# Performance work log

Hardware: AMD Instinct MI355X
Metric: run time of the kernel (lower is better)

Reference implementation:

```python
import jax, jax.numpy as jnp
import numpy as np

EPS = 1e-12  # torch F.normalize clamp
D = 4        # max_displacement


def _l2norm_c(x):
    # L2 normalize over channel dim (axis=1), matching F.normalize(p=2, dim=1)
    n = jnp.sqrt(jnp.sum(x * x, axis=1, keepdims=True))
    return x / jnp.maximum(n, EPS)


def setup_inputs() -> dict:
    key = jax.random.key(0)
    k1, k2 = jax.random.split(key)
    B, C, H, W = 4, 128, 128, 256
    feat1 = jax.random.normal(k1, (B, C, H, W), dtype=jnp.float32)
    feat2_warped = jax.random.normal(k2, (B, C, H, W), dtype=jnp.float32)
    return {"feat1": feat1, "feat2_warped": feat2_warped}


def reference(feat1, feat2_warped):
    B, C, H, W = feat1.shape
    f1 = _l2norm_c(feat1)
    f2 = _l2norm_c(feat2_warped)
    # zero-pad spatial dims by D (matches F.unfold padding=D)
    f2p = jnp.pad(f2, ((0, 0), (0, 0), (D, D), (D, D)))
    costs = []
    # fixed (2D+1)^2 = 81 displacements, row-major (dy, dx) to match unfold ordering
    for dy in range(2 * D + 1):
        for dx in range(2 * D + 1):
            shifted = jax.lax.slice(f2p, (0, 0, dy, dx), (B, C, dy + H, dx + W))
            costs.append(jnp.sum(f1 * shifted, axis=1) / C)  # (B,H,W)
    cost = jnp.stack(costs, axis=1)  # (B, 81, H, W)
    return jax.nn.leaky_relu(cost, negative_slope=0.1)
```

## Files before the change

kernel.cpp:

```cpp
#include <hip/hip_runtime.h>

#define B_ 4
#define C_ 128
#define H_ 128
#define W_ 256
#define HW_ (H_ * W_)
#define ND 81
#define TH 8
#define TW 16
#define HR 16
#define WCOL 32
#define KC 32
#define NCHUNK (C_ / KC)
#define NTHREADS 512

typedef short bf16x8 __attribute__((ext_vector_type(8)));
typedef float f32x4 __attribute__((ext_vector_type(4)));
typedef float f32x4v __attribute__((ext_vector_type(4)));
typedef unsigned int u32x4 __attribute__((ext_vector_type(4)));

__device__ __forceinline__ int swz(int px, int byteInHalf) {
    int r = px >> 1;
    int base = (r << 7) + ((px & 1) << 6) + byteInHalf;
    return base ^ ((r & 7) << 4);
}

__device__ __forceinline__ unsigned int cvt_pk_bf16(float a, float b) {
    unsigned int r;
    asm("v_cvt_pk_bf16_f32 %0, %1, %2" : "=v"(r) : "v"(a), "v"(b));
    return r;
}

__device__ __forceinline__ void dot2_sq(unsigned int u, float& ss) {
    asm("v_dot2_f32_bf16 %0, %1, %1, %0" : "+v"(ss) : "v"(u));
}

#define BARRIER()                                             \
    do {                                                      \
        asm volatile("s_waitcnt lgkmcnt(0)" ::: "memory");    \
        __builtin_amdgcn_s_barrier();                         \
    } while (0)

__global__ __launch_bounds__(NTHREADS)
void corr81_kernel(const float* __restrict__ f1g, const float* __restrict__ f2g,
                   float* __restrict__ out) {
    __shared__ __align__(16) unsigned short f2s[2][HR * WCOL * KC];
    __shared__ __align__(16) unsigned short f1s[2][TH * TW * KC];
    float* invn2 = (float*)&f2s[0][0];
    float* invn1 = (float*)&f1s[0][0];

    const int tid  = threadIdx.x;
    const int lane = tid & 63;
    const int wave = tid >> 6;
    const int col  = lane & 15;
    const int quad = lane >> 4;

    const int flat = blockIdx.x + 16 * blockIdx.y + 256 * blockIdx.z;
    const int orig = (flat & 7) * 128 + (flat >> 3);
    const int w0 = (orig & 15) * TW;
    const int h0 = ((orig >> 4) & 15) * TH;
    const int b  = orig >> 8;
    const size_t inBase = (size_t)b * C_ * HW_;

    const int g2  = tid & 7;
    const int cp2 = (tid >> 3) & 15;
    const int rq  = tid >> 7;
    const int gw2 = w0 - 4 + g2 * 4;
    const bool colok2 = (gw2 >= 0) && (gw2 < W_);

    const int g1  = tid & 3;
    const int cp1 = (tid >> 2) & 15;
    const int r1  = tid >> 6;
    const float* src1 = f1g + inBase + (size_t)(h0 + r1) * W_ + (w0 + g1 * 4);

    const int aOff = swz(wave * 16 + col, quad * 16);

    f32x4 acc[9][2];
#pragma unroll
    for (int d = 0; d < 9; ++d) {
        acc[d][0] = (f32x4)0.f;
        acc[d][1] = (f32x4)0.f;
    }

    float ss2 = 0.f, ss1 = 0.f;
    f32x4v A0[4], A1[4], B0, B1;

#define ISSUE_LOADS(kc0)                                                        \
    {                                                                           \
        _Pragma("unroll")                                                       \
        for (int i = 0; i < 4; ++i) {                                           \
            int r  = i * 4 + rq;                                                \
            int gh = h0 - 4 + r;                                                \
            if (colok2 && gh >= 0 && gh < H_) {                                 \
                const float* s = f2g + inBase + (size_t)((kc0) + cp2 * 2) * HW_ \
                                 + (size_t)gh * W_ + gw2;                       \
                A0[i] = *(const f32x4v*)s;                                      \
                A1[i] = *(const f32x4v*)(s + HW_);                              \
            } else {                                                            \
                A0[i] = (f32x4v)0.f;                                            \
                A1[i] = (f32x4v)0.f;                                            \
            }                                                                   \
        }                                                                       \
        const float* s = src1 + (size_t)((kc0) + cp1 * 2) * HW_;                \
        B0 = *(const f32x4v*)s;                                                 \
        B1 = *(const f32x4v*)(s + HW_);                                         \
    }

#define PACK_WRITE(buf)                                                         \
    {                                                                           \
        char* w2 = (char*)&f2s[(buf)][0];                                       \
        char* w1 = (char*)&f1s[(buf)][0];                                       \
        _Pragma("unroll")                                                       \
        for (int i = 0; i < 4; ++i) {                                           \
            int r = i * 4 + rq;                                                 \
            _Pragma("unroll")                                                   \
            for (int j = 0; j < 4; ++j) {                                       \
                int px = r * 32 + g2 * 4 + j;                                   \
                *(unsigned int*)(w2 + swz(px, cp2 * 4)) =                       \
                    cvt_pk_bf16(A0[i][j], A1[i][j]);                            \
            }                                                                   \
        }                                                                       \
        _Pragma("unroll")                                                       \
        for (int j = 0; j < 4; ++j) {                                           \
            int px = r1 * 16 + g1 * 4 + j;                                      \
            *(unsigned int*)(w1 + swz(px, cp1 * 4)) = cvt_pk_bf16(B0[j], B1[j]);\
        }                                                                       \
    }

#define MFMA_PHASE(buf)                                                         \
    {                                                                           \
        const char* r2 = (const char*)&f2s[(buf)][0];                           \
        const char* r1p = (const char*)&f1s[(buf)][0];                          \
        bf16x8 af = *(const bf16x8*)(r1p + aOff);                               \
        _Pragma("unroll")                                                       \
        for (int dy = 0; dy < 9; ++dy) {                                        \
            int pb = (wave + dy) * WCOL + col;                                  \
            bf16x8 b0 = *(const bf16x8*)(r2 + swz(pb, quad * 16));              \
            bf16x8 b1 = *(const bf16x8*)(r2 + swz(pb + 16, quad * 16));         \
            acc[dy][0] = __builtin_amdgcn_mfma_f32_16x16x32_bf16(af, b0, acc[dy][0], 0, 0, 0); \
            acc[dy][1] = __builtin_amdgcn_mfma_f32_16x16x32_bf16(af, b1, acc[dy][1], 0, 0, 0); \
        }                                                                       \
    }

#define NORM_PHASE(buf)                                                         \
    {                                                                           \
        const char* r2 = (const char*)&f2s[(buf)][0];                           \
        const char* r1p = (const char*)&f1s[(buf)][0];                          \
        _Pragma("unroll")                                                       \
        for (int j = 0; j < 4; ++j) {                                           \
            u32x4 v = *(const u32x4*)(r2 + swz(tid, j * 16));                   \
            dot2_sq(v[0], ss2); dot2_sq(v[1], ss2);                             \
            dot2_sq(v[2], ss2); dot2_sq(v[3], ss2);                             \
        }                                                                       \
        u32x4 v = *(const u32x4*)(r1p + swz(tid >> 2, (tid & 3) * 16));         \
        dot2_sq(v[0], ss1); dot2_sq(v[1], ss1);                                 \
        dot2_sq(v[2], ss1); dot2_sq(v[3], ss1);                                 \
    }

    ISSUE_LOADS(0);
    PACK_WRITE(0);
    ISSUE_LOADS(KC);
    BARRIER();

#pragma unroll
    for (int k = 0; k < NCHUNK; ++k) {
        const int bk = k & 1;
        MFMA_PHASE(bk);
        if (k < NCHUNK - 1) {
            PACK_WRITE(bk ^ 1);
            if (k < NCHUNK - 2) ISSUE_LOADS((k + 2) * KC);
            NORM_PHASE(bk);
        } else {
            NORM_PHASE(bk);
            invn2[tid] = 1.f / fmaxf(sqrtf(ss2), 1e-12f);
            float t1 = ss1 + __shfl_xor(ss1, 1);
            t1 += __shfl_xor(t1, 2);
            if ((tid & 3) == 0) invn1[tid >> 2] = 1.f / fmaxf(sqrtf(t1), 1e-12f);
        }
        BARRIER();
    }

    const int hOut = h0 + wave;
    float* outB = out + (size_t)b * ND * HW_ + (size_t)hOut * W_;
    const float scale = 1.f / (float)C_;

#pragma unroll
    for (int dy = 0; dy < 9; ++dy) {
        int hr = wave + dy;
#pragma unroll
        for (int t = 0; t < 2; ++t) {
            float i2 = invn2[hr * WCOL + t * 16 + col];
#pragma unroll
            for (int r = 0; r < 4; ++r) {
                int row = quad * 4 + r;
                int dx = t * 16 + col - row;
                if (dx >= 0 && dx <= 8) {
                    float v = acc[dy][t][r] * invn1[wave * 16 + row] * i2 * scale;
                    v = (v >= 0.f) ? v : 0.1f * v;
                    outB[(size_t)(dy * 9 + dx) * HW_ + (w0 + row)] = v;
                }
            }
        }
    }
#undef ISSUE_LOADS
#undef PACK_WRITE
#undef MFMA_PHASE
#undef NORM_PHASE
}

extern "C" void kernel_launch(void* const* d_in, const int* in_sizes, int n_in,
                              void* d_out, int out_size, void* d_ws, size_t ws_size,
                              hipStream_t stream) {
    const float* f1 = (const float*)d_in[0];
    const float* f2 = (const float*)d_in[1];
    float* out = (float*)d_out;
    dim3 grid(W_ / TW, H_ / TH, B_);
    corr81_kernel<<<grid, NTHREADS, 0, stream>>>(f1, f2, out);
}
```

Before: 64.18 us.

## Load one pixel per thread across 32 channels and fold norms into packing

Global loads for f2 now give each thread one pixel and all 32 channels of the chunk, replacing the old float4 loads. The thread writes a full 64-byte channel row to LDS with 16-byte stores under a new slot swizzle. Sum-of-squares for the norms is computed from registers during packing, which removes the separate LDS-reading norm phase and its extra LDS traffic. The cost is scalar global loads, which coalesce across lanes along W but issue many more load instructions and need more registers (32 floats per thread in flight). There is also a final extra barrier before the epilogue.

```diff
diff --git a/kernel.cpp b/kernel.cpp
--- a/kernel.cpp
+++ b/kernel.cpp
@@ -13,16 +13,15 @@
 #define KC 32
 #define NCHUNK (C_ / KC)
 #define NTHREADS 512
+#define BUFSZ 40960
+#define F1OFF 32768
 
 typedef short bf16x8 __attribute__((ext_vector_type(8)));
 typedef float f32x4 __attribute__((ext_vector_type(4)));
-typedef float f32x4v __attribute__((ext_vector_type(4)));
 typedef unsigned int u32x4 __attribute__((ext_vector_type(4)));
 
-__device__ __forceinline__ int swz(int px, int byteInHalf) {
-    int r = px >> 1;
-    int base = (r << 7) + ((px & 1) << 6) + byteInHalf;
-    return base ^ ((r & 7) << 4);
+__device__ __forceinline__ int slotswz(int px, int slot) {
+    return px * 64 + ((slot ^ (px & 3) ^ ((px >> 2) & 3)) * 16);
 }
 
 __device__ __forceinline__ unsigned int cvt_pk_bf16(float a, float b) {
@@ -44,10 +43,10 @@
 __global__ __launch_bounds__(NTHREADS)
 void corr81_kernel(const float* __restrict__ f1g, const float* __restrict__ f2g,
                    float* __restrict__ out) {
-    __shared__ __align__(16) unsigned short f2s[2][HR * WCOL * KC];
-    __shared__ __align__(16) unsigned short f1s[2][TH * TW * KC];
-    float* invn2 = (float*)&f2s[0][0];
-    float* invn1 = (float*)&f1s[0][0];
+    __shared__ __align__(16) char lds[2][BUFSZ];
+    char* ldsc = &lds[0][0];
+    float* invn2 = (float*)&lds[0][0];
+    float* invn1 = (float*)&lds[0][2048];
 
     const int tid  = threadIdx.x;
     const int lane = tid & 63;
@@ -60,106 +59,90 @@
     const int w0 = (orig & 15) * TW;
     const int h0 = ((orig >> 4) & 15) * TH;
     const int b  = orig >> 8;
-    const size_t inBase = (size_t)b * C_ * HW_;
-
-    const int g2  = tid & 7;
-    const int cp2 = (tid >> 3) & 15;
-    const int rq  = tid >> 7;
-    const int gw2 = w0 - 4 + g2 * 4;
-    const bool colok2 = (gw2 >= 0) && (gw2 < W_);
-
-    const int g1  = tid & 3;
-    const int cp1 = (tid >> 2) & 15;
-    const int r1  = tid >> 6;
-    const float* src1 = f1g + inBase + (size_t)(h0 + r1) * W_ + (w0 + g1 * 4);
-
-    const int aOff = swz(wave * 16 + col, quad * 16);
+    const float* f2base = f2g + (size_t)b * C_ * HW_;
+    const float* f1base = f1g + (size_t)b * C_ * HW_;
+
+    const int hh2 = tid >> 5, ww2 = tid & 31;
+    const int gh2 = h0 - 4 + hh2, gw2 = w0 - 4 + ww2;
+    const bool v2 = (gh2 >= 0) && (gh2 < H_) && (gw2 >= 0) && (gw2 < W_);
+    const int offs2 = v2 ? (gh2 * W_ + gw2) : 0;
+    int wa[4];
+#pragma unroll
+    for (int s = 0; s < 4; ++s) wa[s] = slotswz(tid, s);
+
+    const int px1w = tid >> 2, q1 = tid & 3;
+    const int offs1 = (h0 + (px1w >> 4)) * W_ + (w0 + (px1w & 15)) + q1 * 8 * HW_;
+    const int w1a = F1OFF + slotswz(px1w, q1);
+
+    const int slotr = (quad ^ (col & 3) ^ ((col >> 2) & 3)) * 16;
+    const int rb2 = wave * 2048 + col * 64 + slotr;
+    const int rb1 = F1OFF + (wave * 16 + col) * 64 + slotr;
 
     f32x4 acc[9][2];
 #pragma unroll
-    for (int d = 0; d < 9; ++d) {
-        acc[d][0] = (f32x4)0.f;
-        acc[d][1] = (f32x4)0.f;
-    }
-
-    float ss2 = 0.f, ss1 = 0.f;
-    f32x4v A0[4], A1[4], B0, B1;
-
-#define ISSUE_LOADS(kc0)                                                        \
-    {                                                                           \
-        _Pragma("unroll")                                                       \
-        for (int i = 0; i < 4; ++i) {                                           \
-            int r  = i * 4 + rq;                                                \
-            int gh = h0 - 4 + r;                                                \
-            if (colok2 && gh >= 0 && gh < H_) {                                 \
-                const float* s = f2g + inBase + (size_t)((kc0) + cp2 * 2) * HW_ \
-                                 + (size_t)gh * W_ + gw2;                       \
-                A0[i] = *(const f32x4v*)s;                                      \
-                A1[i] = *(const f32x4v*)(s + HW_);                              \
-            } else {                                                            \
-                A0[i] = (f32x4v)0.f;                                            \
-                A1[i] = (f32x4v)0.f;                                            \
-            }                                                                   \
+    for (int d = 0; d < 9; ++d) { acc[d][0] = (f32x4)0.f; acc[d][1] = (f32x4)0.f; }
+
+    f32x4 A[8] = {};
+    f32x4 F[2] = {};
+    float ss2a = 0.f, ss2b = 0.f, ss1 = 0.f;
+
+#define ISSUE_F2(kc0)                                                           \
+    if (v2) {                                                                   \
+        _Pragma("unroll")                                                       \
+        for (int c = 0; c < 32; ++c)                                            \
+            A[c >> 2][c & 3] = (f2base + (size_t)((kc0) + c) * HW_)[offs2];     \
+    }
+
+#define ISSUE_F1(kc0)                                                           \
+    {                                                                           \
+        _Pragma("unroll")                                                       \
+        for (int j = 0; j < 8; ++j)                                             \
+            F[j >> 2][j & 3] = (f1base + (size_t)((kc0) + j) * HW_)[offs1];     \
+    }
+
+#define PACK_F2(buf)                                                            \
+    {                                                                           \
+        _Pragma("unroll")                                                       \
+        for (int s = 0; s < 4; ++s) {                                           \
+            u32x4 U;                                                            \
+            U[0] = cvt_pk_bf16(A[s * 2][0], A[s * 2][1]);                       \
+            U[1] = cvt_pk_bf16(A[s * 2][2], A[s * 2][3]);                       \
+            U[2] = cvt_pk_bf16(A[s * 2 + 1][0], A[s * 2 + 1][1]);               \
+            U[3] = cvt_pk_bf16(A[s * 2 + 1][2], A[s * 2 + 1][3]);               \
+            dot2_sq(U[0], ss2a); dot2_sq(U[1], ss2b);                           \
+            dot2_sq(U[2], ss2a); dot2_sq(U[3], ss2b);                           \
+            *(u32x4*)(ldsc + (buf) * BUFSZ + wa[s]) = U;                        \
         }                                                                       \
-        const float* s = src1 + (size_t)((kc0) + cp1 * 2) * HW_;                \
-        B0 = *(const f32x4v*)s;                                                 \
-        B1 = *(const f32x4v*)(s + HW_);                                         \
-    }
-
-#define PACK_WRITE(buf)                                                         \
-    {                                                                           \
-        char* w2 = (char*)&f2s[(buf)][0];                                       \
-        char* w1 = (char*)&f1s[(buf)][0];                                       \
-        _Pragma("unroll")                                                       \
-        for (int i = 0; i < 4; ++i) {                                           \
-            int r = i * 4 + rq;                                                 \
-            _Pragma("unroll")                                                   \
-            for (int j = 0; j < 4; ++j) {                                       \
-                int px = r * 32 + g2 * 4 + j;                                   \
-                *(unsigned int*)(w2 + swz(px, cp2 * 4)) =                       \
-                    cvt_pk_bf16(A0[i][j], A1[i][j]);                            \
-            }                                                                   \
-        }                                                                       \
-        _Pragma("unroll")                                                       \
-        for (int j = 0; j < 4; ++j) {                                           \
-            int px = r1 * 16 + g1 * 4 + j;                                      \
-            *(unsigned int*)(w1 + swz(px, cp1 * 4)) = cvt_pk_bf16(B0[j], B1[j]);\
-        }                                                                       \
+    }
+
+#define PACK_F1(buf)                                                            \
+    {                                                                           \
+        u32x4 U;                                                                \
+        U[0] = cvt_pk_bf16(F[0][0], F[0][1]);                                   \
+        U[1] = cvt_pk_bf16(F[0][2], F[0][3]);                                   \
+        U[2] = cvt_pk_bf16(F[1][0], F[1][1]);                                   \
+        U[3] = cvt_pk_bf16(F[1][2], F[1][3]);                                   \
+        dot2_sq(U[0], ss1); dot2_sq(U[1], ss1);                                 \
+        dot2_sq(U[2], ss1); dot2_sq(U[3], ss1);                                 \
+        *(u32x4*)(ldsc + (buf) * BUFSZ + w1a) = U;                              \
     }
 
 #define MFMA_PHASE(buf)                                                         \
     {                                                                           \
-        const char* r2 = (const char*)&f2s[(buf)][0];                           \
-        const char* r1p = (const char*)&f1s[(buf)][0];                          \
-        bf16x8 af = *(const bf16x8*)(r1p + aOff);                               \
+        const char* rb = ldsc + (buf) * BUFSZ;                                  \
+        bf16x8 af = *(const bf16x8*)(rb + rb1);                                 \
         _Pragma("unroll")                                                       \
         for (int dy = 0; dy < 9; ++dy) {                                        \
-            int pb = (wave + dy) * WCOL + col;                                  \
-            bf16x8 b0 = *(const bf16x8*)(r2 + swz(pb, quad * 16));              \
-            bf16x8 b1 = *(const bf16x8*)(r2 + swz(pb + 16, quad * 16));         \
+            bf16x8 b0 = *(const bf16x8*)(rb + rb2 + dy * 2048);                 \
+            bf16x8 b1 = *(const bf16x8*)(rb + rb2 + dy * 2048 + 1024);          \
             acc[dy][0] = __builtin_amdgcn_mfma_f32_16x16x32_bf16(af, b0, acc[dy][0], 0, 0, 0); \
             acc[dy][1] = __builtin_amdgcn_mfma_f32_16x16x32_bf16(af, b1, acc[dy][1], 0, 0, 0); \
         }                                                                       \
     }
 
-#define NORM_PHASE(buf)                                                         \
-    {                                                                           \
-        const char* r2 = (const char*)&f2s[(buf)][0];                           \
-        const char* r1p = (const char*)&f1s[(buf)][0];                          \
-        _Pragma("unroll")                                                       \
-        for (int j = 0; j < 4; ++j) {                                           \
-            u32x4 v = *(const u32x4*)(r2 + swz(tid, j * 16));                   \
-            dot2_sq(v[0], ss2); dot2_sq(v[1], ss2);                             \
-            dot2_sq(v[2], ss2); dot2_sq(v[3], ss2);                             \
-        }                                                                       \
-        u32x4 v = *(const u32x4*)(r1p + swz(tid >> 2, (tid & 3) * 16));         \
-        dot2_sq(v[0], ss1); dot2_sq(v[1], ss1);                                 \
-        dot2_sq(v[2], ss1); dot2_sq(v[3], ss1);                                 \
-    }
-
-    ISSUE_LOADS(0);
-    PACK_WRITE(0);
-    ISSUE_LOADS(KC);
+    ISSUE_F2(0); ISSUE_F1(0);
+    PACK_F2(0);  PACK_F1(0);
+    ISSUE_F2(KC); ISSUE_F1(KC);
     BARRIER();
 
 #pragma unroll
@@ -167,18 +150,17 @@
         const int bk = k & 1;
         MFMA_PHASE(bk);
         if (k < NCHUNK - 1) {
-            PACK_WRITE(bk ^ 1);
-            if (k < NCHUNK - 2) ISSUE_LOADS((k + 2) * KC);
-            NORM_PHASE(bk);
-        } else {
-            NORM_PHASE(bk);
-            invn2[tid] = 1.f / fmaxf(sqrtf(ss2), 1e-12f);
-            float t1 = ss1 + __shfl_xor(ss1, 1);
-            t1 += __shfl_xor(t1, 2);
-            if ((tid & 3) == 0) invn1[tid >> 2] = 1.f / fmaxf(sqrtf(t1), 1e-12f);
+            PACK_F2(bk ^ 1); PACK_F1(bk ^ 1);
+            if (k < NCHUNK - 2) { ISSUE_F2((k + 2) * KC); ISSUE_F1((k + 2) * KC); }
+            BARRIER();
         }
-        BARRIER();
-    }
+    }
+
+    invn2[tid] = 1.f / fmaxf(sqrtf(ss2a + ss2b), 1e-12f);
+    float t1 = ss1 + __shfl_xor(ss1, 1);
+    t1 += __shfl_xor(t1, 2);
+    if (q1 == 0) invn1[px1w] = 1.f / fmaxf(sqrtf(t1), 1e-12f);
+    BARRIER();
 
     const int hOut = h0 + wave;
     float* outB = out + (size_t)b * ND * HW_ + (size_t)hOut * W_;
@@ -202,10 +184,11 @@
             }
         }
     }
-#undef ISSUE_LOADS
-#undef PACK_WRITE
+#undef ISSUE_F2
+#undef ISSUE_F1
+#undef PACK_F2
+#undef PACK_F1
 #undef MFMA_PHASE
-#undef NORM_PHASE
 }
 
 extern "C" void kernel_launch(void* const* d_in, const int* in_sizes, int n_in,
```

After: 67.92 us. +5.8%, slower.
